# Optimization experiments

Measured on AMD Instinct MI355X. Metric: run time of the kernel, lower is better.

## Reference

```python
import jax, jax.numpy as jnp
import numpy as np

# Dimensions (babyGPT-50m: GPT-2-small-ish)
B, T, V, C, H, L = 2, 1024, 50257, 768, 12, 6
D = C // H
STD = 0.02
EPS = 1e-5


def _normal(k, shape):
    return (jax.random.normal(k, shape, dtype=jnp.float32) * STD)


def setup_inputs() -> dict:
    key = jax.random.key(0)
    ks = jax.random.split(key, 12)
    inp = {
        "idx": jax.random.randint(ks[0], (B, T), 0, V, dtype=jnp.int64 if jax.config.jax_enable_x64 else jnp.int32),
        "tok_emb": _normal(ks[1], (V, C)),
        "pos_emb": _normal(ks[2], (1, T, C)),
        # per-layer params stacked along leading L axis
        "ln1_g": jnp.ones((L, C), jnp.float32),
        "ln1_b": jnp.zeros((L, C), jnp.float32),
        "Wq": _normal(ks[3], (L, C, C)), "bq": jnp.zeros((L, C), jnp.float32),
        "Wk": _normal(ks[4], (L, C, C)), "bk": jnp.zeros((L, C), jnp.float32),
        "Wv": _normal(ks[5], (L, C, C)), "bv": jnp.zeros((L, C), jnp.float32),
        "Wp": _normal(ks[6], (L, C, C)), "bp": jnp.zeros((L, C), jnp.float32),
        "ln2_g": jnp.ones((L, C), jnp.float32),
        "ln2_b": jnp.zeros((L, C), jnp.float32),
        "Wf1": _normal(ks[7], (L, C, 4 * C)), "bf1": jnp.zeros((L, 4 * C), jnp.float32),
        "Wf2": _normal(ks[8], (L, 4 * C, C)), "bf2": jnp.zeros((L, C), jnp.float32),
        "lnf_g": jnp.ones((C,), jnp.float32),
        "lnf_b": jnp.zeros((C,), jnp.float32),
        "head_W": _normal(ks[9], (C, V)),  # head has bias=False
    }
    return inp


def _ln(x, g, b):
    m = jnp.mean(x, axis=-1, keepdims=True)
    v = jnp.var(x, axis=-1, keepdims=True)
    return (x - m) * jax.lax.rsqrt(v + EPS) * g + b


def _gpt_forward(idx, tok_emb, pos_emb, ln1_g, ln1_b, Wq, bq, Wk, bk, Wv, bv,
                 Wp, bp, ln2_g, ln2_b, Wf1, bf1, Wf2, bf2, lnf_g, lnf_b, head_W):
    x = tok_emb[idx] + pos_emb[:, :T]          # [B,T,C]; dropout is identity (eval)
    causal = jnp.tril(jnp.ones((T, T), bool))  # same tril mask as the buffer
    scale = 1.0 / np.sqrt(D).astype(np.float32)

    def block(x, p):
        g1, b1, wq, bq_, wk, bk_, wv, bv_, wp, bp_, g2, b2, w1, b1f, w2, b2f = p
        h = _ln(x, g1, b1)
        q = (h @ wq + bq_).reshape(B, T, H, D)
        k = (h @ wk + bk_).reshape(B, T, H, D)
        v = (h @ wv + bv_).reshape(B, T, H, D)
        att = jnp.einsum('bthd,bshd->bhts', q, k) * scale   # [B,H,T,T]
        att = jnp.where(causal, att, jnp.float32(-10000.0))  # masked_fill value
        att = jax.nn.softmax(att, axis=-1)
        y = jnp.einsum('bhts,bshd->bthd', att, v).reshape(B, T, C)
        x = x + y @ wp + bp_
        h2 = _ln(x, g2, b2)
        ff = jax.nn.gelu(h2 @ w1 + b1f, approximate=False) @ w2 + b2f  # exact GELU, dropout=eval
        return x + ff, None

    layer_params = (ln1_g, ln1_b, Wq, bq, Wk, bk, Wv, bv, Wp, bp,
                    ln2_g, ln2_b, Wf1, bf1, Wf2, bf2)
    x, _ = jax.lax.scan(block, x, layer_params)
    x = _ln(x, lnf_g, lnf_b)
    return x @ head_W  # logits [B,T,V]


def reference(idx, tok_emb, pos_emb, ln1_g, ln1_b, Wq, bq, Wk, bk, Wv, bv,
              Wp, bp, ln2_g, ln2_b, Wf1, bf1, Wf2, bf2, lnf_g, lnf_b, head_W):
    return _gpt_forward(idx, tok_emb, pos_emb, ln1_g, ln1_b, Wq, bq, Wk, bk, Wv, bv,
                        Wp, bp, ln2_g, ln2_b, Wf1, bf1, Wf2, bf2, lnf_g, lnf_b, head_W)
```

## Files before the change

### kernel.cpp

```cpp
#include <hip/hip_runtime.h>
#include <hip/hip_bf16.h>
#include <math.h>

#define Bsz 2
#define Tt 1024
#define Vv 50257
#define Cc 768
#define Hh 12
#define Ll 6
#define NTOK (Bsz*Tt)
#define VPAD 50304

typedef __attribute__((ext_vector_type(8))) short bf16x8;
typedef __attribute__((ext_vector_type(8))) unsigned short u16x8;
typedef __attribute__((ext_vector_type(4))) unsigned short u16x4;
typedef __attribute__((ext_vector_type(4))) float f32x4;
typedef unsigned short u16;

static __device__ __forceinline__ u16 f2bf(float f){
  unsigned u = __float_as_uint(f);
  u += 0x7FFF + ((u >> 16) & 1);
  return (u16)(u >> 16);
}
static __device__ __forceinline__ float bf2f(u16 h){
  return __uint_as_float(((unsigned)h) << 16);
}

#define GL16(g,l) __builtin_amdgcn_global_load_lds( \
    (const __attribute__((address_space(1))) void*)(g), \
    (__attribute__((address_space(3))) void*)(l), 16, 0, 0)
#define WAITVM(n) asm volatile("s_waitcnt vmcnt(%0)" :: "n"(n) : "memory")

__global__ void embed_kernel(const int* __restrict__ idx, const float* __restrict__ tok,
                             const float* __restrict__ pos, float* __restrict__ x){
  const int C4 = Cc/4;
  int i = blockIdx.x * 256 + threadIdx.x;
  if (i >= NTOK*C4) return;
  int tk = i / C4, c4 = i % C4;
  int row = idx[tk];
  int t = tk % Tt;
  float4 a = ((const float4*)tok)[(size_t)row*C4 + c4];
  float4 p = ((const float4*)pos)[(size_t)t*C4 + c4];
  float4 r; r.x=a.x+p.x; r.y=a.y+p.y; r.z=a.z+p.z; r.w=a.w+p.w;
  ((float4*)x)[i] = r;
}

__global__ void ln_kernel(const float* __restrict__ in, const float* __restrict__ g,
                          const float* __restrict__ bt, u16* __restrict__ out){
  int row = blockIdx.x, tid = threadIdx.x;
  const float* r = in + (size_t)row*Cc;
  float v0=r[tid], v1=r[tid+256], v2=r[tid+512];
  float s  = v0+v1+v2;
  float s2 = v0*v0+v1*v1+v2*v2;
  #pragma unroll
  for (int off=32; off; off>>=1){ s += __shfl_xor(s,off); s2 += __shfl_xor(s2,off); }
  __shared__ float red[8];
  int wid = tid >> 6;
  if ((tid & 63) == 0){ red[wid]=s; red[4+wid]=s2; }
  __syncthreads();
  float S  = red[0]+red[1]+red[2]+red[3];
  float S2 = red[4]+red[5]+red[6]+red[7];
  float mean = S * (1.0f/Cc);
  float var  = S2 * (1.0f/Cc) - mean*mean;
  float rstd = rsqrtf(var + 1e-5f);
  u16* o = out + (size_t)row*Cc;
  o[tid]     = f2bf((v0-mean)*rstd*g[tid]     + bt[tid]);
  o[tid+256] = f2bf((v1-mean)*rstd*g[tid+256] + bt[tid+256]);
  o[tid+512] = f2bf((v2-mean)*rstd*g[tid+512] + bt[tid+512]);
}

__global__ void wtrans_kernel(const float* __restrict__ in, u16* __restrict__ out,
                              int K, int N, int Npad, size_t lsi, size_t lso){
  __shared__ float t[64][33];
  const float* inp = in + (size_t)blockIdx.z*lsi;
  u16* op = out + (size_t)blockIdx.z*lso;
  int n0 = blockIdx.x*32, k0 = blockIdx.y*64;
  int tx = threadIdx.x, ty = threadIdx.y;
  #pragma unroll
  for (int i=0;i<8;i++){
    int k = k0+ty+i*8, n = n0+tx;
    t[ty+i*8][tx] = (n < N) ? inp[(size_t)k*N + n] : 0.f;
  }
  __syncthreads();
  #pragma unroll
  for (int i=0;i<2;i++){
    int nl = i*16 + ty*2 + (tx>>4);
    int kl = (tx&15)*4;
    int n = n0 + nl;
    if (n < Npad){
      u16x4 pk;
      pk[0] = f2bf(t[kl+0][nl]); pk[1] = f2bf(t[kl+1][nl]);
      pk[2] = f2bf(t[kl+2][nl]); pk[3] = f2bf(t[kl+3][nl]);
      *(u16x4*)&op[(size_t)n*K + k0 + kl] = pk;
    }
  }
}

__global__ void vtrans_kernel(const u16* __restrict__ qkv, u16* __restrict__ vT){
  __shared__ u16 s[32][33];
  int bh = blockIdx.z; int b = bh/Hh, h = bh - b*Hh;
  int t0 = blockIdx.x*32, d0 = blockIdx.y*32;
  int tx=threadIdx.x, ty=threadIdx.y;
  #pragma unroll
  for (int i=0;i<4;i++)
    s[ty+i*8][tx] = qkv[(size_t)(b*Tt + t0+ty+i*8)*2304 + 1536 + h*64 + d0 + tx];
  __syncthreads();
  #pragma unroll
  for (int i=0;i<4;i++)
    vT[((size_t)bh*64 + d0+ty+i*8)*Tt + t0 + tx] = s[tx][ty+i*8];
}

__global__ void bconcat_kernel(const float* __restrict__ bq, const float* __restrict__ bk,
                               const float* __restrict__ bv, float* __restrict__ o){
  int i = blockIdx.x*256 + threadIdx.x;
  if (i >= Ll*2304) return;
  int l = i/2304, j = i - l*2304;
  o[i] = (j < 768) ? bq[l*768+j] : (j < 1536) ? bk[l*768+j-768] : bv[l*768+j-1536];
}

__global__ __launch_bounds__(256) void flash_kernel(
    const u16* __restrict__ qkv, const u16* __restrict__ vT, u16* __restrict__ y){
  __shared__ u16 Ks[2][64*64];
  __shared__ u16 Vs[2][64*64];
  __shared__ u16 Ps[4][16*64];
  int bx = blockIdx.x;
  int bh = blockIdx.y; int b = bh/Hh, h = bh - b*Hh;
  int q0 = bx*64;
  int tid = threadIdx.x, lane = tid&63, wid = tid>>6;
  const size_t tokbase = (size_t)b*Tt;
  int arow = lane&15, akof = (lane>>4)*8;
  bf16x8 qa[2];
  #pragma unroll
  for (int ks=0;ks<2;ks++)
    qa[ks] = *(const bf16x8*)&qkv[(tokbase + q0 + wid*16 + arow)*2304
                                  + h*64 + ks*32 + akof];
  int srow = lane>>3;
  int sbyte = ((lane&7)*16) ^ (srow<<4);
  const u16* kbase = qkv + tokbase*2304 + 768 + h*64;
  const u16* vbase = vT + (size_t)bh*64*Tt;
  auto STAGEKV = [&](int t, int bb){
    int j0 = t*64;
    #pragma unroll
    for (int c=0;c<2;c++){
      int r = wid*16 + c*8 + srow;
      GL16(kbase + (size_t)(j0 + r)*2304 + (sbyte>>1), &Ks[bb][(wid*16 + c*8)*64]);
      GL16(vbase + (size_t)r*Tt + j0 + (sbyte>>1),     &Vs[bb][(wid*16 + c*8)*64]);
    }
  };
  float m_r[4], l_r[4];
  f32x4 o_acc[4] = {};
  #pragma unroll
  for (int jj=0;jj<4;jj++){ m_r[jj] = -1e30f; l_r[jj] = 0.f; }

  int njt = bx + 1;
  STAGEKV(0, 0);
  asm volatile("s_waitcnt vmcnt(0)" ::: "memory");
  __builtin_amdgcn_s_barrier();
  for (int t=0; t<njt; t++){
    int cur = t&1;
    if (t+1 < njt) STAGEKV(t+1, cur^1);
    int j0 = t*64;
    f32x4 sacc[4] = {};
    #pragma unroll
    for (int ks=0;ks<2;ks++){
      bf16x8 kf[4];
      #pragma unroll
      for (int ni=0;ni<4;ni++){
        int s16 = ni*16 + (lane&15);
        int kb = (ks*64 + (lane>>4)*16) ^ ((s16&7)<<4);
        kf[ni] = *(const bf16x8*)((const char*)&Ks[cur][0] + s16*128 + kb);
      }
      #pragma unroll
      for (int ni=0;ni<4;ni++)
        sacc[ni] = __builtin_amdgcn_mfma_f32_16x16x32_bf16(qa[ks], kf[ni], sacc[ni], 0,0,0);
    }
    float tmax[4];
    #pragma unroll
    for (int jj=0;jj<4;jj++) tmax[jj] = -1e30f;
    #pragma unroll
    for (int ni=0;ni<4;ni++)
      #pragma unroll
      for (int jj=0;jj<4;jj++){
        float v = sacc[ni][jj]*0.125f;
        int sg = j0 + ni*16 + (lane&15);
        int tg = q0 + wid*16 + (lane>>4)*4 + jj;
        v = (sg <= tg) ? v : -1e30f;
        sacc[ni][jj] = v;
        tmax[jj] = fmaxf(tmax[jj], v);
      }
    #pragma unroll
    for (int jj=0;jj<4;jj++){
      float tm = tmax[jj];
      tm = fmaxf(tm, __shfl_xor(tm,1)); tm = fmaxf(tm, __shfl_xor(tm,2));
      tm = fmaxf(tm, __shfl_xor(tm,4)); tm = fmaxf(tm, __shfl_xor(tm,8));
      float mn = fmaxf(m_r[jj], tm);
      float al = __expf(m_r[jj] - mn);
      m_r[jj] = mn;
      l_r[jj] *= al;
      tmax[jj] = al;
    }
    float tsum[4] = {};
    #pragma unroll
    for (int ni=0;ni<4;ni++)
      #pragma unroll
      for (int jj=0;jj<4;jj++){
        float p = __expf(sacc[ni][jj] - m_r[jj]);
        tsum[jj] += p;
        int pr = (lane>>4)*4 + jj;
        int pcb = (2*(ni*16 + (lane&15))) ^ ((pr&7)<<4);
        *(u16*)((char*)&Ps[wid][0] + pr*128 + pcb) = f2bf(p);
      }
    #pragma unroll
    for (int jj=0;jj<4;jj++){
      float ts = tsum[jj];
      ts += __shfl_xor(ts,1); ts += __shfl_xor(ts,2);
      ts += __shfl_xor(ts,4); ts += __shfl_xor(ts,8);
      l_r[jj] += ts;
      float al = tmax[jj];
      #pragma unroll
      for (int ni2=0;ni2<4;ni2++) o_acc[ni2][jj] *= al;
    }
    #pragma unroll
    for (int ks2=0;ks2<2;ks2++){
      bf16x8 pa, vf[4];
      int prr = lane&15;
      int pb = (ks2*64 + (lane>>4)*16) ^ ((prr&7)<<4);
      pa = *(const bf16x8*)((const char*)&Ps[wid][0] + prr*128 + pb);
      #pragma unroll
      for (int ni2=0;ni2<4;ni2++){
        int d16 = ni2*16 + (lane&15);
        int sb = (ks2*64 + (lane>>4)*16) ^ ((d16&7)<<4);
        vf[ni2] = *(const bf16x8*)((const char*)&Vs[cur][0] + d16*128 + sb);
      }
      #pragma unroll
      for (int ni2=0;ni2<4;ni2++)
        o_acc[ni2] = __builtin_amdgcn_mfma_f32_16x16x32_bf16(pa, vf[ni2], o_acc[ni2], 0,0,0);
    }
    asm volatile("s_waitcnt vmcnt(0) lgkmcnt(0)" ::: "memory");
    __builtin_amdgcn_s_barrier();
  }
  #pragma unroll
  for (int jj=0;jj<4;jj++){
    float inv = 1.0f / l_r[jj];
    int tok2 = q0 + wid*16 + (lane>>4)*4 + jj;
    size_t rb = (tokbase + tok2)*Cc + h*64;
    #pragma unroll
    for (int ni2=0;ni2<4;ni2++)
      y[rb + ni2*16 + (lane&15)] = f2bf(o_acc[ni2][jj] * inv);
  }
}

template<int NBUF, int BM, int BN, bool BIAS, bool RESID, bool GELU, bool OUTBF, bool ROWSCAN>
__global__ __launch_bounds__(256) void mm_kernel(
    const u16* __restrict__ A, const u16* __restrict__ Bm,
    const float* __restrict__ bias, const float* __restrict__ resid,
    void* __restrict__ out, int N, int K, int lda, int ldb, int ldc)
{
  constexpr int FM   = BM/32;
  constexpr int FN   = BN/32;
  constexpr int CPW  = FN*16;
  constexpr int ESTR = CPW + 4;
  constexpr int ABUF = BM*32;
  constexpr int BBUF = BN*32;
  constexpr int LOADS = (BM+BN)/64;
  constexpr int SMEM_STAGE = NBUF*(ABUF+BBUF)*2;
  constexpr int SMEM_EPI   = 4*16*ESTR*4;
  constexpr int SMEMB = SMEM_STAGE > SMEM_EPI ? SMEM_STAGE : SMEM_EPI;
  __shared__ __align__(16) char smem[SMEMB];
  u16* As = (u16*)smem;
  u16* Bs = As + NBUF*ABUF;

  int bx = blockIdx.x, by = blockIdx.y;
  {
    int gx = gridDim.x;
    int nwg = gx * gridDim.y;
    int flat = by*gx + bx;
    int qq = nwg >> 3, rr = nwg & 7;
    int xcd = flat & 7, lid = flat >> 3;
    int swz = (xcd < rr) ? xcd*(qq+1) + lid : rr*(qq+1) + (xcd-rr)*qq + lid;
    bx = swz % gx; by = swz / gx;
  }
  int m0 = bx*BM, n0 = by*BN;
  int tid = threadIdx.x, lane = tid & 63, wid = tid >> 6;
  int wr = wid >> 1, wc = wid & 1;
  int r0 = wr*(BM/2), c0 = wc*(BN/2);
  int lrow = lane & 15, koff = (lane >> 4)*8;
  int sr = lane >> 2, sk = (lane & 3)*8;
  const u16* Ap = A + (size_t)(m0 + wid*(BM/4) + sr)*lda + sk;
  const u16* Bp = Bm + (size_t)(n0 + wid*(BN/4) + sr)*ldb + sk;
  int nt = K/32;
  auto STAGE = [&](int t, int bb){
    int kk = t*32;
    u16* Al = As + bb*ABUF + wid*(ABUF/4);
    GL16(Ap + kk, Al);
    if constexpr (BM==128) GL16(Ap + kk + (size_t)16*lda, Al + 512);
    u16* Bl = Bs + bb*BBUF + wid*(BBUF/4);
    GL16(Bp + kk, Bl);
    if constexpr (BN==128) GL16(Bp + kk + (size_t)16*ldb, Bl + 512);
  };
  f32x4 acc[FM][FN] = {};
  if constexpr (NBUF==2){
    STAGE(0, 0);
    WAITVM(0);
    __builtin_amdgcn_s_barrier();
  } else {
    STAGE(0, 0);
    if (nt > 1) STAGE(1, 1);
    WAITVM(LOADS);
    __builtin_amdgcn_s_barrier();
  }
  for (int t = 0; t < nt; t++){
    int bb = (NBUF==2) ? (t & 1) : (t % 3);
    if constexpr (NBUF==2){
      if (t+1 < nt) STAGE(t+1, (t+1)&1);
    } else {
      if (t+2 < nt) STAGE(t+2, (t+2)%3);
    }
    const u16* Ab2 = As + bb*ABUF;
    const u16* Bb2 = Bs + bb*BBUF;
    bf16x8 af[FM], bfr[FN];
    #pragma unroll
    for (int m=0;m<FM;m++) af[m] = *(const bf16x8*)&Ab2[(r0 + m*16 + lrow)*32 + koff];
    #pragma unroll
    for (int n=0;n<FN;n++) bfr[n] = *(const bf16x8*)&Bb2[(c0 + n*16 + lrow)*32 + koff];
    #pragma unroll
    for (int m=0;m<FM;m++)
      #pragma unroll
      for (int n=0;n<FN;n++)
        acc[m][n] = __builtin_amdgcn_mfma_f32_16x16x32_bf16(af[m], bfr[n], acc[m][n], 0,0,0);
    if constexpr (NBUF==2){
      asm volatile("s_waitcnt vmcnt(0) lgkmcnt(0)" ::: "memory");
    } else {
      if (t+2 < nt) WAITVM(LOADS); else WAITVM(0);
    }
    __builtin_amdgcn_s_barrier();
  }

  float* ebuf = (float*)smem + wid*16*ESTR;
  int er = lane >> 2;
  int ec = (lane & 3) * (CPW/4);
  #pragma unroll
  for (int m=0;m<FM;m++){
    #pragma unroll
    for (int n=0;n<FN;n++)
      #pragma unroll
      for (int j=0;j<4;j++)
        ebuf[((lane>>4)*4+j)*ESTR + n*16 + (lane&15)] = acc[m][n][j];
    __builtin_amdgcn_s_waitcnt(0);
    if constexpr (ROWSCAN){
      #pragma unroll
      for (int rr2=0; rr2<16; rr2++){
        int gr2 = m0 + r0 + m*16 + rr2;
        int gc2 = n0 + c0 + lane;
        float v = ebuf[rr2*ESTR + lane];
        if (gc2 < N)
          __builtin_nontemporal_store(v, &((float*)out)[(size_t)gr2*ldc + gc2]);
      }
    } else {
      int grow = m0 + r0 + m*16 + er;
      int gcol = n0 + c0 + ec;
      size_t rbase = (size_t)grow*ldc;
      if constexpr (OUTBF){
        u16 tmp[CPW/4];
        #pragma unroll
        for (int q=0;q<FN;q++){
          float4 v = *(const float4*)&ebuf[er*ESTR + ec + q*4];
          float f0=v.x, f1=v.y, f2=v.z, f3=v.w;
          if (BIAS){
            float4 b4 = *(const float4*)&bias[gcol + q*4];
            f0+=b4.x; f1+=b4.y; f2+=b4.z; f3+=b4.w;
          }
          if (GELU){
            f0 = 0.5f*f0*(1.f+erff(f0*0.70710678118654752f));
            f1 = 0.5f*f1*(1.f+erff(f1*0.70710678118654752f));
            f2 = 0.5f*f2*(1.f+erff(f2*0.70710678118654752f));
            f3 = 0.5f*f3*(1.f+erff(f3*0.70710678118654752f));
          }
          tmp[q*4+0]=f2bf(f0); tmp[q*4+1]=f2bf(f1);
          tmp[q*4+2]=f2bf(f2); tmp[q*4+3]=f2bf(f3);
        }
        #pragma unroll
        for (int s2=0; s2<CPW/32; s2++)
          *(u16x8*)&((u16*)out)[rbase + gcol + s2*8] = *(const u16x8*)&tmp[s2*8];
      } else {
        #pragma unroll
        for (int q=0;q<FN;q++){
          float4 v = *(const float4*)&ebuf[er*ESTR + ec + q*4];
          float f0=v.x, f1=v.y, f2=v.z, f3=v.w;
          if (BIAS){
            float4 b4 = *(const float4*)&bias[gcol + q*4];
            f0+=b4.x; f1+=b4.y; f2+=b4.z; f3+=b4.w;
          }
          if (GELU){
            f0 = 0.5f*f0*(1.f+erff(f0*0.70710678118654752f));
            f1 = 0.5f*f1*(1.f+erff(f1*0.70710678118654752f));
            f2 = 0.5f*f2*(1.f+erff(f2*0.70710678118654752f));
            f3 = 0.5f*f3*(1.f+erff(f3*0.70710678118654752f));
          }
          if (RESID){
            float4 r4 = *(const float4*)&resid[rbase + gcol + q*4];
            f0+=r4.x; f1+=r4.y; f2+=r4.z; f3+=r4.w;
          }
          float4 o4; o4.x=f0; o4.y=f1; o4.z=f2; o4.w=f3;
          *(float4*)&((float*)out)[rbase + gcol + q*4] = o4;
        }
      }
    }
  }
}

extern "C" void kernel_launch(void* const* d_in, const int* in_sizes, int n_in,
                              void* d_out, int out_size, void* d_ws, size_t ws_size,
                              hipStream_t stream){
  const int*   idx  = (const int*)d_in[0];
  const float* tok  = (const float*)d_in[1];
  const float* pos  = (const float*)d_in[2];
  const float* ln1g = (const float*)d_in[3];
  const float* ln1b = (const float*)d_in[4];
  const float* Wq   = (const float*)d_in[5];
  const float* bq   = (const float*)d_in[6];
  const float* Wk   = (const float*)d_in[7];
  const float* bk   = (const float*)d_in[8];
  const float* Wv   = (const float*)d_in[9];
  const float* bv   = (const float*)d_in[10];
  const float* Wp   = (const float*)d_in[11];
  const float* bp   = (const float*)d_in[12];
  const float* ln2g = (const float*)d_in[13];
  const float* ln2b = (const float*)d_in[14];
  const float* Wf1  = (const float*)d_in[15];
  const float* bf1  = (const float*)d_in[16];
  const float* Wf2  = (const float*)d_in[17];
  const float* bf2  = (const float*)d_in[18];
  const float* lnfg = (const float*)d_in[19];
  const float* lnfb = (const float*)d_in[20];
  const float* headW= (const float*)d_in[21];
  float* outp = (float*)d_out;

  char* w = (char*)d_ws;
  u16* wqkvT = (u16*)w;  w += (size_t)Ll*2304*768*2;
  u16* wpT   = (u16*)w;  w += (size_t)Ll*768*768*2;
  u16* wf1T  = (u16*)w;  w += (size_t)Ll*3072*768*2;
  u16* wf2T  = (u16*)w;  w += (size_t)Ll*768*3072*2;
  u16* headT = (u16*)w;  w += (size_t)VPAD*768*2;
  float* bqkv= (float*)w;w += (size_t)Ll*2304*4;
  float* x   = (float*)w;w += (size_t)NTOK*Cc*4;
  u16* h     = (u16*)w;  w += (size_t)NTOK*Cc*2;
  u16* qkv   = (u16*)w;  w += (size_t)NTOK*2304*2;
  u16* vT    = (u16*)w;  w += (size_t)Bsz*Hh*64*Tt*2;
  u16* y     = (u16*)w;  w += (size_t)NTOK*Cc*2;
  u16* ff    = (u16*)w;  w += (size_t)NTOK*4*Cc*2;

  dim3 tb(32,8);
  wtrans_kernel<<<dim3(24,12,Ll), tb, 0, stream>>>(Wq, wqkvT,          768, 768, 768, (size_t)Cc*Cc, (size_t)2304*768);
  wtrans_kernel<<<dim3(24,12,Ll), tb, 0, stream>>>(Wk, wqkvT+768*768,  768, 768, 768, (size_t)Cc*Cc, (size_t)2304*768);
  wtrans_kernel<<<dim3(24,12,Ll), tb, 0, stream>>>(Wv, wqkvT+1536*768, 768, 768, 768, (size_t)Cc*Cc, (size_t)2304*768);
  wtrans_kernel<<<dim3(24,12,Ll), tb, 0, stream>>>(Wp, wpT,            768, 768, 768, (size_t)Cc*Cc, (size_t)768*768);
  wtrans_kernel<<<dim3(96,12,Ll), tb, 0, stream>>>(Wf1, wf1T,          768, 3072, 3072, (size_t)Cc*4*Cc, (size_t)3072*768);
  wtrans_kernel<<<dim3(24,48,Ll), tb, 0, stream>>>(Wf2, wf2T,          3072, 768, 768, (size_t)4*Cc*Cc, (size_t)768*3072);
  wtrans_kernel<<<dim3(VPAD/32,12,1), tb, 0, stream>>>(headW, headT, 768, Vv, VPAD, 0, 0);
  bconcat_kernel<<<(Ll*2304+255)/256, 256, 0, stream>>>(bq, bk, bv, bqkv);

  embed_kernel<<<NTOK*(Cc/4)/256, 256, 0, stream>>>(idx, tok, pos, x);

  for (int l=0;l<Ll;l++){
    ln_kernel<<<NTOK, 256, 0, stream>>>(x, ln1g+l*Cc, ln1b+l*Cc, h);
    mm_kernel<3,64,128,true,false,false,true,false><<<dim3(32,18,1), 256, 0, stream>>>(
        h, wqkvT+(size_t)l*2304*768, bqkv+l*2304, nullptr, qkv, 2304, 768, 768, 768, 2304);
    vtrans_kernel<<<dim3(32,2,Bsz*Hh), tb, 0, stream>>>(qkv, vT);
    flash_kernel<<<dim3(Tt/64, Bsz*Hh), 256, 0, stream>>>(qkv, vT, y);
    mm_kernel<3,64,64,true,true,false,false,false><<<dim3(32,12,1), 256, 0, stream>>>(
        y, wpT+(size_t)l*768*768, bp+l*Cc, x, x, 768, 768, 768, 768, 768);
    ln_kernel<<<NTOK, 256, 0, stream>>>(x, ln2g+l*Cc, ln2b+l*Cc, h);
    mm_kernel<3,64,128,true,false,true,true,false><<<dim3(32,24,1), 256, 0, stream>>>(
        h, wf1T+(size_t)l*3072*768, bf1+(size_t)l*4*Cc, nullptr, ff, 3072, 768, 768, 768, 3072);
    mm_kernel<3,64,64,true,true,false,false,false><<<dim3(32,12,1), 256, 0, stream>>>(
        ff, wf2T+(size_t)l*768*3072, bf2+l*Cc, x, x, 768, 3072, 3072, 3072, 768);
  }
  ln_kernel<<<NTOK, 256, 0, stream>>>(x, lnfg, lnfb, h);
  mm_kernel<2,128,128,false,false,false,false,true><<<dim3(16,VPAD/128,1), 256, 0, stream>>>(
      h, headT, nullptr, nullptr, outp, Vv, 768, 768, 768, Vv);
}
```

Measured before the change: 1.249 ms.

## Double GEMM K-tile to 64 with XOR-swizzled LDS layout

The GEMM kernel now stages K=64 per iteration instead of 32, so it runs half as many loop iterations and barriers. The LDS layout is XOR-swizzled on 16-byte chunks to avoid bank conflicts when fragments are read at the wider 128-byte row stride. The QKV and FC1 GEMMs drop from triple to double buffering so the larger stages still fit in shared memory. The cost is less prefetch depth for those two GEMMs and more LDS per block, which may lower occupancy.

```diff
diff --git a/kernel.cpp b/kernel.cpp
--- a/kernel.cpp
+++ b/kernel.cpp
@@ -260,9 +260,11 @@
   constexpr int FN   = BN/32;
   constexpr int CPW  = FN*16;
   constexpr int ESTR = CPW + 4;
-  constexpr int ABUF = BM*32;
-  constexpr int BBUF = BN*32;
-  constexpr int LOADS = (BM+BN)/64;
+  constexpr int ABUF = BM*64;
+  constexpr int BBUF = BN*64;
+  constexpr int ACALLS = BM/32;
+  constexpr int BCALLS = BN/32;
+  constexpr int LOADS = ACALLS + BCALLS;
   constexpr int SMEM_STAGE = NBUF*(ABUF+BBUF)*2;
   constexpr int SMEM_EPI   = 4*16*ESTR*4;
   constexpr int SMEMB = SMEM_STAGE > SMEM_EPI ? SMEM_STAGE : SMEM_EPI;
@@ -284,19 +286,23 @@
   int tid = threadIdx.x, lane = tid & 63, wid = tid >> 6;
   int wr = wid >> 1, wc = wid & 1;
   int r0 = wr*(BM/2), c0 = wc*(BN/2);
-  int lrow = lane & 15, koff = (lane >> 4)*8;
-  int sr = lane >> 2, sk = (lane & 3)*8;
-  const u16* Ap = A + (size_t)(m0 + wid*(BM/4) + sr)*lda + sk;
-  const u16* Bp = Bm + (size_t)(n0 + wid*(BN/4) + sr)*ldb + sk;
-  int nt = K/32;
+  int lrow = lane & 15;
+  int sswz = ((lane & 7) ^ (lane >> 3)) * 8;
+  const u16* Ap = A + (size_t)(m0 + wid*(BM/4) + (lane>>3))*lda + sswz;
+  const u16* Bp = Bm + (size_t)(n0 + wid*(BN/4) + (lane>>3))*ldb + sswz;
+  int cof0 = (((lane>>4)    ) ^ (lane&7)) << 4;
+  int cof1 = (((lane>>4) + 4) ^ (lane&7)) << 4;
+  int nt = K/64;
   auto STAGE = [&](int t, int bb){
-    int kk = t*32;
-    u16* Al = As + bb*ABUF + wid*(ABUF/4);
-    GL16(Ap + kk, Al);
-    if constexpr (BM==128) GL16(Ap + kk + (size_t)16*lda, Al + 512);
-    u16* Bl = Bs + bb*BBUF + wid*(BBUF/4);
-    GL16(Bp + kk, Bl);
-    if constexpr (BN==128) GL16(Bp + kk + (size_t)16*ldb, Bl + 512);
+    int kk = t*64;
+    u16* Albase = As + bb*ABUF + (wid*(BM/4))*64;
+    #pragma unroll
+    for (int c=0;c<ACALLS;c++)
+      GL16(Ap + kk + (size_t)(c*8)*lda, Albase + c*512);
+    u16* Blbase = Bs + bb*BBUF + (wid*(BN/4))*64;
+    #pragma unroll
+    for (int c=0;c<BCALLS;c++)
+      GL16(Bp + kk + (size_t)(c*8)*ldb, Blbase + c*512);
   };
   f32x4 acc[FM][FN] = {};
   if constexpr (NBUF==2){
@@ -316,18 +322,22 @@
     } else {
       if (t+2 < nt) STAGE(t+2, (t+2)%3);
     }
-    const u16* Ab2 = As + bb*ABUF;
-    const u16* Bb2 = Bs + bb*BBUF;
-    bf16x8 af[FM], bfr[FN];
-    #pragma unroll
-    for (int m=0;m<FM;m++) af[m] = *(const bf16x8*)&Ab2[(r0 + m*16 + lrow)*32 + koff];
-    #pragma unroll
-    for (int n=0;n<FN;n++) bfr[n] = *(const bf16x8*)&Bb2[(c0 + n*16 + lrow)*32 + koff];
-    #pragma unroll
-    for (int m=0;m<FM;m++)
-      #pragma unroll
-      for (int n=0;n<FN;n++)
-        acc[m][n] = __builtin_amdgcn_mfma_f32_16x16x32_bf16(af[m], bfr[n], acc[m][n], 0,0,0);
+    const char* Ab2 = (const char*)(As + bb*ABUF);
+    const char* Bb2 = (const char*)(Bs + bb*BBUF);
+    #pragma unroll
+    for (int ks=0;ks<2;ks++){
+      int cof = ks ? cof1 : cof0;
+      bf16x8 af[FM], bfr[FN];
+      #pragma unroll
+      for (int m=0;m<FM;m++) af[m] = *(const bf16x8*)(Ab2 + (r0 + m*16 + lrow)*128 + cof);
+      #pragma unroll
+      for (int n=0;n<FN;n++) bfr[n] = *(const bf16x8*)(Bb2 + (c0 + n*16 + lrow)*128 + cof);
+      #pragma unroll
+      for (int m=0;m<FM;m++)
+        #pragma unroll
+        for (int n=0;n<FN;n++)
+          acc[m][n] = __builtin_amdgcn_mfma_f32_16x16x32_bf16(af[m], bfr[n], acc[m][n], 0,0,0);
+    }
     if constexpr (NBUF==2){
       asm volatile("s_waitcnt vmcnt(0) lgkmcnt(0)" ::: "memory");
     } else {
@@ -464,14 +474,14 @@
 
   for (int l=0;l<Ll;l++){
     ln_kernel<<<NTOK, 256, 0, stream>>>(x, ln1g+l*Cc, ln1b+l*Cc, h);
-    mm_kernel<3,64,128,true,false,false,true,false><<<dim3(32,18,1), 256, 0, stream>>>(
+    mm_kernel<2,64,128,true,false,false,true,false><<<dim3(32,18,1), 256, 0, stream>>>(
         h, wqkvT+(size_t)l*2304*768, bqkv+l*2304, nullptr, qkv, 2304, 768, 768, 768, 2304);
     vtrans_kernel<<<dim3(32,2,Bsz*Hh), tb, 0, stream>>>(qkv, vT);
     flash_kernel<<<dim3(Tt/64, Bsz*Hh), 256, 0, stream>>>(qkv, vT, y);
     mm_kernel<3,64,64,true,true,false,false,false><<<dim3(32,12,1), 256, 0, stream>>>(
         y, wpT+(size_t)l*768*768, bp+l*Cc, x, x, 768, 768, 768, 768, 768);
     ln_kernel<<<NTOK, 256, 0, stream>>>(x, ln2g+l*Cc, ln2b+l*Cc, h);
-    mm_kernel<3,64,128,true,false,true,true,false><<<dim3(32,24,1), 256, 0, stream>>>(
+    mm_kernel<2,64,128,true,false,true,true,false><<<dim3(32,24,1), 256, 0, stream>>>(
         h, wf1T+(size_t)l*3072*768, bf1+(size_t)l*4*Cc, nullptr, ff, 3072, 768, 768, 768, 3072);
     mm_kernel<3,64,64,true,true,false,false,false><<<dim3(32,12,1), 256, 0, stream>>>(
         ff, wf2T+(size_t)l*768*3072, bf2+l*Cc, x, x, 768, 3072, 3072, 3072, 768);
```

Result: faster. 1.148 ms (-8.1%).
